# Kernel tuning notes

Hardware: AMD Instinct MI355X
Metric: run time of the kernel (lower is better)

Reference implementation:

```python
import jax, jax.numpy as jnp
import numpy as np
import math

N, C, L, D = 8, 16, 1024, 7   # x: [N, in_heads=C, L, in_features=D]
H = 16                        # out_heads
SZ = C * D                    # 112 (in_sz == out_sz since in_heads == out_heads)

def setup_inputs() -> dict:
    key = jax.random.key(0)
    ks = jax.random.split(key, 7)
    s = 1.0 / math.sqrt(SZ)
    return {
        "x":  jax.random.normal(ks[0], (N, C, L, D), dtype=jnp.float32),
        "Wq": jax.random.normal(ks[1], (SZ, SZ), dtype=jnp.float32) * s,
        "bq": jax.random.normal(ks[2], (SZ,), dtype=jnp.float32) * s,
        "Wk": jax.random.normal(ks[3], (SZ, SZ), dtype=jnp.float32) * s,
        "bk": jax.random.normal(ks[4], (SZ,), dtype=jnp.float32) * s,
        "Wv": jax.random.normal(ks[5], (SZ, SZ), dtype=jnp.float32) * s,
        "bv": jax.random.normal(ks[6], (SZ,), dtype=jnp.float32) * s,
    }

def _split_heads(t):
    # [N, L, H*d] -> [N, H, L, d]
    n, l, _ = t.shape
    return t.reshape(n, l, H, -1).transpose(0, 2, 1, 3)

def reference(x, Wq, bq, Wk, bk, Wv, bv):
    n, c, l, d = x.shape
    # [N, C, L, D] -> [N, L, C*D]
    xf = x.transpose(0, 2, 1, 3).reshape(n, l, c * d)
    q = _split_heads(xf @ Wq.T + bq)   # [N, H, L, d]
    k = _split_heads(xf @ Wk.T + bk)
    v = _split_heads(xf @ Wv.T + bv)
    scores = jnp.einsum('bhqd,bhkd->bhqk', q, k)
    # NOTE: original scales by sqrt(scores.shape[-1]) == sqrt(L), not sqrt(head_dim)
    scores = scores / jnp.sqrt(jnp.asarray(l, scores.dtype))
    weights = jax.nn.softmax(scores.astype(jnp.float32), axis=-1).astype(scores.dtype)
    # dropout p=0.5 is identity in eval mode
    return jnp.einsum('bhqk,bhkd->bhqd', weights, v)
```

## Files before the change

### kernel.cpp

```cpp
#include <hip/hip_runtime.h>
#include <math.h>

#define NB 8
#define CH 16
#define LL 1024
#define DD 7
#define HH 16

typedef float  v4f __attribute__((ext_vector_type(4)));
typedef short  v8s __attribute__((ext_vector_type(8)));

#if __has_builtin(__builtin_amdgcn_exp2f)
#define EXP2F(x) __builtin_amdgcn_exp2f(x)
#else
#define EXP2F(x) exp2f(x)
#endif

__device__ inline unsigned bf16_rne(float f) {
    unsigned u = __builtin_bit_cast(unsigned, f);
    return (u + 0x7fffu + ((u >> 16) & 1u)) >> 16;
}
__device__ inline unsigned pack_trunc(float a, float b) {
    unsigned ua = __builtin_bit_cast(unsigned, a);
    unsigned ub = __builtin_bit_cast(unsigned, b);
    return (ua >> 16) | (ub & 0xffff0000u);
}

__global__ __launch_bounds__(256, 2) void qkv_proj(
    const float* __restrict__ x,
    const float* __restrict__ Wq, const float* __restrict__ bq,
    const float* __restrict__ Wk, const float* __restrict__ bk,
    const float* __restrict__ Wv, const float* __restrict__ bv,
    unsigned short* __restrict__ qkvb)
{
    __shared__ __align__(16) float Ws[112 * 112];
    __shared__ __align__(16) float xt[64 * 116];

    int bx  = blockIdx.x;
    int mat = bx / (NB * 16);
    int rem = bx % (NB * 16);
    int n   = rem / 16;
    int l0  = (rem % 16) * 64;

    const float* W = (mat == 0) ? Wq : (mat == 1) ? Wk : Wv;
    const float* b = (mat == 0) ? bq : (mat == 1) ? bk : bv;

    int tid = threadIdx.x;

    for (int idx = tid; idx < 112 * 112; idx += 256) Ws[idx] = W[idx];
    for (int idx = tid; idx < 64 * 112; idx += 256) {
        int c  = idx / 448;
        int r  = idx - c * 448;
        int l  = r / 7;
        int dd = r - l * 7;
        xt[l * 116 + c * 7 + dd] = x[((n * CH + c) * LL + l0 + l) * DD + dd];
    }
    __syncthreads();

    int jh = tid >> 4;
    int lg = tid & 15;

    float acc[4][7];
    #pragma unroll
    for (int j = 0; j < 7; ++j) {
        float bj = b[jh * 7 + j];
        #pragma unroll
        for (int r = 0; r < 4; ++r) acc[r][j] = bj;
    }

    for (int i4 = 0; i4 < 28; ++i4) {
        float4 wv[7];
        #pragma unroll
        for (int j = 0; j < 7; ++j)
            wv[j] = *(const float4*)&Ws[(jh * 7 + j) * 112 + i4 * 4];
        #pragma unroll
        for (int r = 0; r < 4; ++r) {
            float4 xv = *(const float4*)&xt[(r * 16 + lg) * 116 + i4 * 4];
            #pragma unroll
            for (int j = 0; j < 7; ++j) {
                acc[r][j] += xv.x * wv[j].x;
                acc[r][j] += xv.y * wv[j].y;
                acc[r][j] += xv.z * wv[j].z;
                acc[r][j] += xv.w * wv[j].w;
            }
        }
    }

    const float scale = (mat == 0) ? 0.0450842200277801f  : 1.0f;
    #pragma unroll
    for (int r = 0; r < 4; ++r) {
        int row = l0 + r * 16 + lg;
        unsigned d0 = bf16_rne(acc[r][0] * scale) | (bf16_rne(acc[r][1] * scale) << 16);
        unsigned d1 = bf16_rne(acc[r][2] * scale) | (bf16_rne(acc[r][3] * scale) << 16);
        unsigned d2 = bf16_rne(acc[r][4] * scale) | (bf16_rne(acc[r][5] * scale) << 16);
        unsigned d3 = bf16_rne(acc[r][6] * scale);
        uint4* dst = (uint4*)qkvb + (((size_t)(mat * NB + n) * HH + jh) * LL + row);
        *dst = make_uint4(d0, d1, d2, d3);
    }
}

__global__ __launch_bounds__(256, 2) void attn(
    const unsigned short* __restrict__ qkvb, float* __restrict__ out)
{
    __shared__ __align__(16) unsigned short sm[(16384 + 16512 + 20480) / 2];
    unsigned short* Kl = sm;
    unsigned short* Vt = sm + 8192;
    unsigned short* Pb = sm + 8192 + 8256;

    int bx = blockIdx.x;
    int qt = bx & 3, h = (bx >> 2) & 15, n = bx >> 6;
    int tid  = threadIdx.x;
    int wave = tid >> 6, lane = tid & 63, l15 = lane & 15, l4 = lane >> 4;

    const unsigned short* Qg = qkvb + (size_t)((0 * NB + n) * HH + h) * (LL * 8);
    const unsigned short* Kg = qkvb + (size_t)((1 * NB + n) * HH + h) * (LL * 8);
    const unsigned short* Vg = qkvb + (size_t)((2 * NB + n) * HH + h) * (LL * 8);

    {
        const uint4* Ks = (const uint4*)Kg;
        const uint4* Vs = (const uint4*)Vg;
        uint4* Kd = (uint4*)Kl;
        uint4* Vd = (uint4*)Pb;
        for (int i = tid; i < LL; i += 256) { Kd[i] = Ks[i]; Vd[i] = Vs[i]; }
    }
    __syncthreads();

    {
        const uint4* Vd = (const uint4*)Pb;
        uint4 r0 = Vd[4 * tid + 0], r1 = Vd[4 * tid + 1];
        uint4 r2 = Vd[4 * tid + 2], r3 = Vd[4 * tid + 3];
        const unsigned* p0 = (const unsigned*)&r0;
        const unsigned* p1 = (const unsigned*)&r1;
        const unsigned* p2 = (const unsigned*)&r2;
        const unsigned* p3 = (const unsigned*)&r3;
        #pragma unroll
        for (int d = 0; d < 7; ++d) {
            unsigned a0 = p0[d >> 1], a1 = p1[d >> 1], a2 = p2[d >> 1], a3 = p3[d >> 1];
            unsigned w0, w1;
            if (d & 1) { w0 = (a0 >> 16) | (a1 & 0xffff0000u); w1 = (a2 >> 16) | (a3 & 0xffff0000u); }
            else       { w0 = (a0 & 0xffffu) | (a1 << 16);     w1 = (a2 & 0xffffu) | (a3 << 16); }
            *(uint2*)&Vt[d * 1032 + 4 * tid] = make_uint2(w0, w1);
        }
        *(uint2*)&Vt[7 * 1032 + 4 * tid] = make_uint2(0x3f803f80u, 0x3f803f80u);
    }
    __syncthreads();

    int qbase = qt * 256 + wave * 64;
    v8s zero8 = {0, 0, 0, 0, 0, 0, 0, 0};

    v8s qf[4];
    #pragma unroll
    for (int t = 0; t < 4; ++t)
        qf[t] = (lane < 16) ? *(const v8s*)(Qg + (size_t)(qbase + t * 16 + l15) * 8) : zero8;

    v4f acc[4];
    #pragma unroll
    for (int t = 0; t < 4; ++t) acc[t] = (v4f){0.f, 0.f, 0.f, 0.f};

    unsigned short* Pw = Pb + wave * 2560;

    for (int c = 0; c < 32; ++c) {
        #pragma unroll
        for (int s = 0; s < 2; ++s) {
            v8s kf = (lane < 16) ? *(const v8s*)(Kl + (c * 32 + s * 16 + l15) * 8) : zero8;
            #pragma unroll
            for (int t = 0; t < 4; ++t) {
                v4f sc = __builtin_amdgcn_mfma_f32_16x16x32_bf16(
                             kf, qf[t], (v4f){0.f, 0.f, 0.f, 0.f}, 0, 0, 0);
                float e0 = EXP2F(sc[0]), e1 = EXP2F(sc[1]);
                float e2 = EXP2F(sc[2]), e3 = EXP2F(sc[3]);
                unsigned w0 = pack_trunc(e0, e1), w1 = pack_trunc(e2, e3);
                *(uint2*)&Pw[(t * 16 + l15) * 40 + s * 16 + l4 * 4] = make_uint2(w0, w1);
            }
        }
        v8s vf = (l15 < 8) ? *(const v8s*)(Vt + l15 * 1032 + c * 32 + l4 * 8) : zero8;
        #pragma unroll
        for (int t = 0; t < 4; ++t) {
            v8s pf = *(const v8s*)&Pw[(t * 16 + l15) * 40 + l4 * 8];
            acc[t] = __builtin_amdgcn_mfma_f32_16x16x32_bf16(pf, vf, acc[t], 0, 0, 0);
        }
    }

    size_t obase = (size_t)(n * HH + h) * LL * 7;
    #pragma unroll
    for (int t = 0; t < 4; ++t) {
        #pragma unroll
        for (int r = 0; r < 4; ++r) {
            float val = acc[t][r];
            float rs  = __shfl(val, 7, 16);
            if (l15 < 7)
                out[obase + (size_t)(qbase + t * 16 + l4 * 4 + r) * 7 + l15] = val / rs;
        }
    }
}

extern "C" void kernel_launch(void* const* d_in, const int* in_sizes, int n_in,
                              void* d_out, int out_size, void* d_ws, size_t ws_size,
                              hipStream_t stream) {
    const float* x  = (const float*)d_in[0];
    const float* Wq = (const float*)d_in[1];
    const float* bq = (const float*)d_in[2];
    const float* Wk = (const float*)d_in[3];
    const float* bk = (const float*)d_in[4];
    const float* Wv = (const float*)d_in[5];
    const float* bv = (const float*)d_in[6];
    unsigned short* qkvb = (unsigned short*)d_ws;
    float* o = (float*)d_out;

    qkv_proj<<<dim3(3 * NB * 16), dim3(256), 0, stream>>>(x, Wq, bq, Wk, bk, Wv, bv, qkvb);
    attn<<<dim3(NB * HH * 4), dim3(256), 0, stream>>>(qkvb, o);
}
```

Baseline: 115.7 us.

## Use 32x32x16 MFMA for QK scores and packed-FMA projection

The attention kernel now computes score tiles with 32x32x16 bf16 MFMAs, two per 32-key chunk instead of eight 16x16x32 ones. It writes exponentiated probabilities as wider 16-byte LDS stores, and the V transpose is permuted with a new row stride to match the new P layout. The projection kernel switches to packed two-wide float FMAs, vectorizes the weight copy into shared memory, and partially unrolls the attention loop. The aim is fewer MFMA issues and less VALU and LDS overhead per chunk, at the cost of a more intricate P/V column mapping whose correctness depends on matching the MFMA output layout.

```diff
diff --git a/kernel.cpp b/kernel.cpp
--- a/kernel.cpp
+++ b/kernel.cpp
@@ -7,8 +7,10 @@
 #define DD 7
 #define HH 16
 
-typedef float  v4f __attribute__((ext_vector_type(4)));
-typedef short  v8s __attribute__((ext_vector_type(8)));
+typedef float  v2f  __attribute__((ext_vector_type(2)));
+typedef float  v4f  __attribute__((ext_vector_type(4)));
+typedef float  v16f __attribute__((ext_vector_type(16)));
+typedef short  v8s  __attribute__((ext_vector_type(8)));
 
 #if __has_builtin(__builtin_amdgcn_exp2f)
 #define EXP2F(x) __builtin_amdgcn_exp2f(x)
@@ -47,7 +49,11 @@
 
     int tid = threadIdx.x;
 
-    for (int idx = tid; idx < 112 * 112; idx += 256) Ws[idx] = W[idx];
+    {
+        const uint4* src = (const uint4*)W;
+        uint4* dst = (uint4*)Ws;
+        for (int i = tid; i < 3136; i += 256) dst[i] = src[i];
+    }
     for (int idx = tid; idx < 64 * 112; idx += 256) {
         int c  = idx / 448;
         int r  = idx - c * 448;
@@ -60,57 +66,71 @@
     int jh = tid >> 4;
     int lg = tid & 15;
 
-    float acc[4][7];
+    v2f acc2[2][7];
     #pragma unroll
     for (int j = 0; j < 7; ++j) {
         float bj = b[jh * 7 + j];
-        #pragma unroll
-        for (int r = 0; r < 4; ++r) acc[r][j] = bj;
-    }
+        acc2[0][j] = (v2f){bj, bj};
+        acc2[1][j] = (v2f){bj, bj};
+    }
+
+    const v4f* Wv4 = (const v4f*)Ws;
+    const v4f* Xv4 = (const v4f*)xt;
 
     for (int i4 = 0; i4 < 28; ++i4) {
-        float4 wv[7];
-        #pragma unroll
-        for (int j = 0; j < 7; ++j)
-            wv[j] = *(const float4*)&Ws[(jh * 7 + j) * 112 + i4 * 4];
-        #pragma unroll
-        for (int r = 0; r < 4; ++r) {
-            float4 xv = *(const float4*)&xt[(r * 16 + lg) * 116 + i4 * 4];
+        v4f wv[7];
+        #pragma unroll
+        for (int j = 0; j < 7; ++j) wv[j] = Wv4[(jh * 7 + j) * 28 + i4];
+        v4f x0 = Xv4[(0  + lg) * 29 + i4];
+        v4f x1 = Xv4[(16 + lg) * 29 + i4];
+        v4f x2 = Xv4[(32 + lg) * 29 + i4];
+        v4f x3 = Xv4[(48 + lg) * 29 + i4];
+        #pragma unroll
+        for (int f = 0; f < 4; ++f) {
+            v2f xa = (v2f){x0[f], x1[f]};
+            v2f xb = (v2f){x2[f], x3[f]};
             #pragma unroll
             for (int j = 0; j < 7; ++j) {
-                acc[r][j] += xv.x * wv[j].x;
-                acc[r][j] += xv.y * wv[j].y;
-                acc[r][j] += xv.z * wv[j].z;
-                acc[r][j] += xv.w * wv[j].w;
+                v2f wj = (v2f){wv[j][f], wv[j][f]};
+                acc2[0][j] += xa * wj;
+                acc2[1][j] += xb * wj;
             }
         }
     }
 
     const float scale = (mat == 0) ? 0.0450842200277801f  : 1.0f;
     #pragma unroll
-    for (int r = 0; r < 4; ++r) {
-        int row = l0 + r * 16 + lg;
-        unsigned d0 = bf16_rne(acc[r][0] * scale) | (bf16_rne(acc[r][1] * scale) << 16);
-        unsigned d1 = bf16_rne(acc[r][2] * scale) | (bf16_rne(acc[r][3] * scale) << 16);
-        unsigned d2 = bf16_rne(acc[r][4] * scale) | (bf16_rne(acc[r][5] * scale) << 16);
-        unsigned d3 = bf16_rne(acc[r][6] * scale);
-        uint4* dst = (uint4*)qkvb + (((size_t)(mat * NB + n) * HH + jh) * LL + row);
-        *dst = make_uint4(d0, d1, d2, d3);
+    for (int rp = 0; rp < 2; ++rp) {
+        #pragma unroll
+        for (int e = 0; e < 2; ++e) {
+            int r = rp * 2 + e;
+            float a0 = acc2[rp][0][e] * scale, a1 = acc2[rp][1][e] * scale;
+            float a2 = acc2[rp][2][e] * scale, a3 = acc2[rp][3][e] * scale;
+            float a4 = acc2[rp][4][e] * scale, a5 = acc2[rp][5][e] * scale;
+            float a6 = acc2[rp][6][e] * scale;
+            unsigned d0 = bf16_rne(a0) | (bf16_rne(a1) << 16);
+            unsigned d1 = bf16_rne(a2) | (bf16_rne(a3) << 16);
+            unsigned d2 = bf16_rne(a4) | (bf16_rne(a5) << 16);
+            unsigned d3 = bf16_rne(a6);
+            int row = l0 + r * 16 + lg;
+            uint4* dst = (uint4*)qkvb + ((size_t)(mat * NB + n) * HH + jh) * LL + row;
+            *dst = make_uint4(d0, d1, d2, d3);
+        }
     }
 }
 
 __global__ __launch_bounds__(256, 2) void attn(
     const unsigned short* __restrict__ qkvb, float* __restrict__ out)
 {
-    __shared__ __align__(16) unsigned short sm[(16384 + 16512 + 20480) / 2];
-    unsigned short* Kl = sm;
-    unsigned short* Vt = sm + 8192;
-    unsigned short* Pb = sm + 8192 + 8256;
+    __shared__ __align__(16) unsigned short Kl[LL * 8];
+    __shared__ __align__(16) unsigned short Vt[8 * 1040];
+    __shared__ __align__(16) unsigned short Pb[4 * 64 * 40];
 
     int bx = blockIdx.x;
     int qt = bx & 3, h = (bx >> 2) & 15, n = bx >> 6;
     int tid  = threadIdx.x;
-    int wave = tid >> 6, lane = tid & 63, l15 = lane & 15, l4 = lane >> 4;
+    int wave = tid >> 6, lane = tid & 63;
+    int l31 = lane & 31, g5 = lane >> 5, l15 = lane & 15, l4 = lane >> 4;
 
     const unsigned short* Qg = qkvb + (size_t)((0 * NB + n) * HH + h) * (LL * 8);
     const unsigned short* Kg = qkvb + (size_t)((1 * NB + n) * HH + h) * (LL * 8);
@@ -121,75 +141,97 @@
         const uint4* Vs = (const uint4*)Vg;
         uint4* Kd = (uint4*)Kl;
         uint4* Vd = (uint4*)Pb;
-        for (int i = tid; i < LL; i += 256) { Kd[i] = Ks[i]; Vd[i] = Vs[i]; }
+        #pragma unroll
+        for (int it = 0; it < 4; ++it) {
+            int i = tid + it * 256;
+            Kd[i] = Ks[i];
+            Vd[i] = Vs[i];
+        }
     }
     __syncthreads();
 
     {
         const uint4* Vd = (const uint4*)Pb;
-        uint4 r0 = Vd[4 * tid + 0], r1 = Vd[4 * tid + 1];
+        uint4 r0 = Vd[4 * tid], r1 = Vd[4 * tid + 1];
         uint4 r2 = Vd[4 * tid + 2], r3 = Vd[4 * tid + 3];
         const unsigned* p0 = (const unsigned*)&r0;
         const unsigned* p1 = (const unsigned*)&r1;
         const unsigned* p2 = (const unsigned*)&r2;
         const unsigned* p3 = (const unsigned*)&r3;
+        int col = ((tid >> 3) << 5) + ((tid & 1) << 4) + (((tid >> 1) & 3) << 2);
         #pragma unroll
         for (int d = 0; d < 7; ++d) {
             unsigned a0 = p0[d >> 1], a1 = p1[d >> 1], a2 = p2[d >> 1], a3 = p3[d >> 1];
             unsigned w0, w1;
             if (d & 1) { w0 = (a0 >> 16) | (a1 & 0xffff0000u); w1 = (a2 >> 16) | (a3 & 0xffff0000u); }
             else       { w0 = (a0 & 0xffffu) | (a1 << 16);     w1 = (a2 & 0xffffu) | (a3 << 16); }
-            *(uint2*)&Vt[d * 1032 + 4 * tid] = make_uint2(w0, w1);
-        }
-        *(uint2*)&Vt[7 * 1032 + 4 * tid] = make_uint2(0x3f803f80u, 0x3f803f80u);
+            *(uint2*)&Vt[d * 1040 + col] = make_uint2(w0, w1);
+        }
+        *(uint2*)&Vt[7 * 1040 + col] = make_uint2(0x3f803f80u, 0x3f803f80u);
     }
     __syncthreads();
 
     int qbase = qt * 256 + wave * 64;
     v8s zero8 = {0, 0, 0, 0, 0, 0, 0, 0};
-
-    v8s qf[4];
-    #pragma unroll
-    for (int t = 0; t < 4; ++t)
-        qf[t] = (lane < 16) ? *(const v8s*)(Qg + (size_t)(qbase + t * 16 + l15) * 8) : zero8;
+    v8s qf0 = (lane < 32) ? *(const v8s*)(Qg + (size_t)(qbase + l31) * 8)      : zero8;
+    v8s qf1 = (lane < 32) ? *(const v8s*)(Qg + (size_t)(qbase + 32 + l31) * 8) : zero8;
 
     v4f acc[4];
     #pragma unroll
-    for (int t = 0; t < 4; ++t) acc[t] = (v4f){0.f, 0.f, 0.f, 0.f};
-
-    unsigned short* Pw = Pb + wave * 2560;
-
+    for (int st = 0; st < 4; ++st) acc[st] = (v4f){0.f, 0.f, 0.f, 0.f};
+
+    unsigned short* Pw = Pb + wave * (64 * 40);
+
+    #pragma unroll 2
     for (int c = 0; c < 32; ++c) {
-        #pragma unroll
-        for (int s = 0; s < 2; ++s) {
-            v8s kf = (lane < 16) ? *(const v8s*)(Kl + (c * 32 + s * 16 + l15) * 8) : zero8;
-            #pragma unroll
-            for (int t = 0; t < 4; ++t) {
-                v4f sc = __builtin_amdgcn_mfma_f32_16x16x32_bf16(
-                             kf, qf[t], (v4f){0.f, 0.f, 0.f, 0.f}, 0, 0, 0);
-                float e0 = EXP2F(sc[0]), e1 = EXP2F(sc[1]);
-                float e2 = EXP2F(sc[2]), e3 = EXP2F(sc[3]);
-                unsigned w0 = pack_trunc(e0, e1), w1 = pack_trunc(e2, e3);
-                *(uint2*)&Pw[(t * 16 + l15) * 40 + s * 16 + l4 * 4] = make_uint2(w0, w1);
-            }
-        }
-        v8s vf = (l15 < 8) ? *(const v8s*)(Vt + l15 * 1032 + c * 32 + l4 * 8) : zero8;
-        #pragma unroll
-        for (int t = 0; t < 4; ++t) {
-            v8s pf = *(const v8s*)&Pw[(t * 16 + l15) * 40 + l4 * 8];
-            acc[t] = __builtin_amdgcn_mfma_f32_16x16x32_bf16(pf, vf, acc[t], 0, 0, 0);
+        v8s kf = (lane < 32) ? *(const v8s*)(Kl + (c * 32 + l31) * 8) : zero8;
+        v16f s0 = __builtin_amdgcn_mfma_f32_32x32x16_bf16(kf, qf0, (v16f){}, 0, 0, 0);
+        v16f s1 = __builtin_amdgcn_mfma_f32_32x32x16_bf16(kf, qf1, (v16f){}, 0, 0, 0);
+        {
+            unsigned short* dst = Pw + l31 * 40 + (g5 << 4);
+            uint4 wa, wb;
+            wa.x = pack_trunc(EXP2F(s0[0]),  EXP2F(s0[1]));
+            wa.y = pack_trunc(EXP2F(s0[2]),  EXP2F(s0[3]));
+            wa.z = pack_trunc(EXP2F(s0[4]),  EXP2F(s0[5]));
+            wa.w = pack_trunc(EXP2F(s0[6]),  EXP2F(s0[7]));
+            wb.x = pack_trunc(EXP2F(s0[8]),  EXP2F(s0[9]));
+            wb.y = pack_trunc(EXP2F(s0[10]), EXP2F(s0[11]));
+            wb.z = pack_trunc(EXP2F(s0[12]), EXP2F(s0[13]));
+            wb.w = pack_trunc(EXP2F(s0[14]), EXP2F(s0[15]));
+            *(uint4*)dst       = wa;
+            *(uint4*)(dst + 8) = wb;
+        }
+        {
+            unsigned short* dst = Pw + (32 + l31) * 40 + (g5 << 4);
+            uint4 wa, wb;
+            wa.x = pack_trunc(EXP2F(s1[0]),  EXP2F(s1[1]));
+            wa.y = pack_trunc(EXP2F(s1[2]),  EXP2F(s1[3]));
+            wa.z = pack_trunc(EXP2F(s1[4]),  EXP2F(s1[5]));
+            wa.w = pack_trunc(EXP2F(s1[6]),  EXP2F(s1[7]));
+            wb.x = pack_trunc(EXP2F(s1[8]),  EXP2F(s1[9]));
+            wb.y = pack_trunc(EXP2F(s1[10]), EXP2F(s1[11]));
+            wb.z = pack_trunc(EXP2F(s1[12]), EXP2F(s1[13]));
+            wb.w = pack_trunc(EXP2F(s1[14]), EXP2F(s1[15]));
+            *(uint4*)dst       = wa;
+            *(uint4*)(dst + 8) = wb;
+        }
+        v8s vf = (l15 < 8) ? *(const v8s*)(Vt + l15 * 1040 + c * 32 + l4 * 8) : zero8;
+        #pragma unroll
+        for (int st = 0; st < 4; ++st) {
+            v8s pf = *(const v8s*)(Pw + (st * 16 + l15) * 40 + l4 * 8);
+            acc[st] = __builtin_amdgcn_mfma_f32_16x16x32_bf16(pf, vf, acc[st], 0, 0, 0);
         }
     }
 
     size_t obase = (size_t)(n * HH + h) * LL * 7;
     #pragma unroll
-    for (int t = 0; t < 4; ++t) {
+    for (int st = 0; st < 4; ++st) {
         #pragma unroll
         for (int r = 0; r < 4; ++r) {
-            float val = acc[t][r];
+            float val = acc[st][r];
             float rs  = __shfl(val, 7, 16);
             if (l15 < 7)
-                out[obase + (size_t)(qbase + t * 16 + l4 * 4 + r) * 7 + l15] = val / rs;
+                out[obase + (size_t)(qbase + st * 16 + l4 * 4 + r) * 7 + l15] = val / rs;
         }
     }
 }
```

New measurement: 110.4 us. -4.6%, faster.
